# Kernel optimization log

Hardware: AMD Instinct MI355X
Metric: run time of the kernel (lower is better)

## Reference

```python
import jax, jax.numpy as jnp
import numpy as np

B, S, M = 8, 2048, 256
D = 512          # input/memory feature dim
P = 512          # proj_dim
H = 8            # num_heads


def setup_inputs() -> dict:
    key = jax.random.key(0)
    ks = jax.random.split(key, 10)
    sc = 0.02
    return {
        "input_seq": jax.random.normal(ks[0], (B, S, D), jnp.float32),
        "memory_cells": jax.random.normal(ks[1], (B, M, D), jnp.float32),
        "Wk": jax.random.normal(ks[2], (D, P), jnp.float32) * sc,
        "bk": jnp.zeros((P,), jnp.float32),
        "Wv": jax.random.normal(ks[3], (D, P), jnp.float32) * sc,
        "bv": jnp.zeros((P,), jnp.float32),
        "Wq": jax.random.normal(ks[4], (H, D, P), jnp.float32) * sc,  # stacked per-head query Dense
        "bq": jnp.zeros((H, P), jnp.float32),
        "Wo": jax.random.normal(ks[5], (H * P, P), jnp.float32) * sc,
        "bo": jnp.zeros((P,), jnp.float32),
    }


def reference(input_seq, memory_cells, Wk, bk, Wv, bv, Wq, bq, Wo, bo):
    # shared key/value projections (multi-query: one K/V for all heads)
    ik = input_seq @ Wk + bk          # [B,S,P]
    mk = memory_cells @ Wk + bk       # [B,M,P]
    iv = input_seq @ Wv + bv          # [B,S,P]
    mv = memory_cells @ Wv + bv       # [B,M,P]

    # per-head queries from memory cells, all heads at once
    q = jnp.einsum('bmd,hdp->bhmp', memory_cells, Wq) + bq[None, :, None, :]  # [B,H,M,P]

    input_score = jnp.einsum('bhmp,bsp->bhms', q, ik)          # [B,H,M,S]
    self_score = jnp.sum(q * mk[:, None], axis=-1, keepdims=True)  # [B,H,M,1]
    score = jnp.concatenate([self_score, input_score], axis=-1)    # [B,H,M,S+1]
    score = score / jnp.sqrt(jnp.float32(P))
    attn = jax.nn.softmax(score, axis=-1)

    self_attn = attn[..., 0:1]                                  # [B,H,M,1]
    input_attn = attn[..., 1:]                                  # [B,H,M,S]
    val = jnp.einsum('bhms,bsp->bhmp', input_attn, iv) + self_attn * mv[:, None]

    # concat heads: [B,M,H*P]
    concat = jnp.transpose(val, (0, 2, 1, 3)).reshape(B, M, H * P)
    return concat @ Wo + bo           # [B,M,P]
```

## Files before the change

### kernel.cpp

```cpp
#include <hip/hip_runtime.h>

#define B_ 8
#define S_ 2048
#define M_ 256
#define D_ 512
#define P_ 512
#define H_ 8

#define SCALE 0.044194173824159216f

typedef __attribute__((ext_vector_type(8))) short bf16x8;
typedef __attribute__((ext_vector_type(4))) float f32x4;

static __device__ __forceinline__ float bf2f(short u) {
  union { float f; unsigned int i; } x;
  x.i = ((unsigned int)(unsigned short)u) << 16;
  return x.f;
}
static __device__ __forceinline__ short f2bf(float f) {
  union { float f; unsigned int i; } x;
  x.f = f;
  unsigned int r = (x.i + 0x7FFFu + ((x.i >> 16) & 1u)) >> 16;
  return (short)r;
}

static __device__ __forceinline__ void gll16(const short* g, short* l) {
  __builtin_amdgcn_global_load_lds(
      (const __attribute__((address_space(1))) void*)g,
      (__attribute__((address_space(3))) void*)l, 16, 0, 0);
}

#define LGKM_WAIT() asm volatile("s_waitcnt lgkmcnt(0)" ::: "memory")
#define VMLG_WAIT() asm volatile("s_waitcnt vmcnt(0) lgkmcnt(0)" ::: "memory")
#define RAW_BAR() do { asm volatile("" ::: "memory"); __builtin_amdgcn_s_barrier(); asm volatile("" ::: "memory"); } while (0)

__global__ __launch_bounds__(256) void cast_both(
    const float* __restrict__ inA, short* __restrict__ outA, int n4A,
    const float* __restrict__ inM, short* __restrict__ outM)
{
  int idx = blockIdx.x * 256 + threadIdx.x;
  const float* in = inA;
  short* out = outA;
  if (idx >= n4A) { idx -= n4A; in = inM; out = outM; }
  float4 v = ((const float4*)in)[idx];
  short o0 = f2bf(v.x), o1 = f2bf(v.y), o2 = f2bf(v.z), o3 = f2bf(v.w);
  uint2 pk;
  pk.x = (unsigned int)(unsigned short)o0 | ((unsigned int)(unsigned short)o1 << 16);
  pk.y = (unsigned int)(unsigned short)o2 | ((unsigned int)(unsigned short)o3 << 16);
  ((uint2*)out)[idx] = pk;
}

__global__ __launch_bounds__(256) void wtrans_all(
    const float* __restrict__ Wk, const float* __restrict__ Wv,
    const float* __restrict__ Wq,
    short* __restrict__ WkT, short* __restrict__ WvT, short* __restrict__ WqT)
{
  __shared__ float tile[32][33];
  const int t = threadIdx.x, tx = t & 31, ty = t >> 5;
  const int z = blockIdx.z;
  const float* inp;
  short* outp;
  if (z == 0)      { inp = Wk; outp = WkT; }
  else if (z == 1) { inp = Wv; outp = WvT; }
  else             { inp = Wq + (size_t)(z - 2) * 512 * 512;
                     outp = WqT + (size_t)(z - 2) * 512 * 512; }
  const int n0 = blockIdx.x * 32, k0 = blockIdx.y * 32;
#pragma unroll
  for (int i = 0; i < 4; ++i)
    tile[ty + 8 * i][tx] = inp[(size_t)(k0 + ty + 8 * i) * 512 + n0 + tx];
  __syncthreads();
#pragma unroll
  for (int i = 0; i < 4; ++i)
    outp[(size_t)(n0 + ty + 8 * i) * 512 + k0 + tx] = f2bf(tile[tx][ty + 8 * i]);
}

__global__ __launch_bounds__(256) void wtrans_wo(
    const float* __restrict__ in, short* __restrict__ out)
{
  __shared__ float tile[32][33];
  const int t = threadIdx.x, tx = t & 31, ty = t >> 5;
  const int n0 = blockIdx.x * 32, k0 = blockIdx.y * 32;
#pragma unroll
  for (int i = 0; i < 4; ++i)
    tile[ty + 8 * i][tx] = in[(size_t)(k0 + ty + 8 * i) * 512 + n0 + tx];
  __syncthreads();
#pragma unroll
  for (int i = 0; i < 4; ++i)
    out[(size_t)(n0 + ty + 8 * i) * 4096 + k0 + tx] = f2bf(tile[tx][ty + 8 * i]);
}

template<int MODE, int K, int N, int LDA, int LDB>
__global__ __launch_bounds__(256, 3) void gemm128(
    const short* __restrict__ Abase, const short* __restrict__ Bbase,
    const float* __restrict__ bias, void* __restrict__ Cv,
    const size_t aZ, const size_t bZ, const size_t cZ,
    float* __restrict__ Ls,
    const float* __restrict__ eselfp, const short* __restrict__ mvbp)
{
  __shared__ short As[4096];
  __shared__ short Bs[4096];
  const int t = threadIdx.x;
  const int w = t >> 6, lane = t & 63, qd = lane >> 4, ln = lane & 15;
  const int wm = (w & 1) * 64, wn = (w >> 1) * 64;

  const int n0 = blockIdx.x * 128;
  const int m0 = blockIdx.y * 128;
  const int z = blockIdx.z;
  const int bsel = z;

  const short* A  = Abase + (size_t)z * aZ;
  const short* Bp = Bbase + (size_t)bsel * bZ;

  const int rr = t >> 2, g0 = t & 3;
  const int gs0 = g0 ^ ((rr >> 1) & 3);
  const int gs1 = g0 ^ (((rr + 64) >> 1) & 3);
  const short* ga0 = A + (size_t)(m0 + rr) * LDA + gs0 * 8;
  const short* ga1 = A + (size_t)(m0 + rr + 64) * LDA + gs1 * 8;
  const short* gb0 = Bp + (size_t)(n0 + rr) * LDB + gs0 * 8;
  const short* gb1 = Bp + (size_t)(n0 + rr + 64) * LDB + gs1 * 8;

  int aoff[4], boff[4];
#pragma unroll
  for (int mt = 0; mt < 4; ++mt) {
    int r = wm + mt * 16 + ln;
    aoff[mt] = r * 32 + (qd ^ ((r >> 1) & 3)) * 8;
  }
#pragma unroll
  for (int nt = 0; nt < 4; ++nt) {
    int r = wn + nt * 16 + ln;
    boff[nt] = r * 32 + (qd ^ ((r >> 1) & 3)) * 8;
  }

  f32x4 acc[4][4];
#pragma unroll
  for (int mt = 0; mt < 4; ++mt)
#pragma unroll
    for (int nt = 0; nt < 4; ++nt) acc[mt][nt] = (f32x4){0.f, 0.f, 0.f, 0.f};

  for (int kc = 0; kc < K; kc += 32) {
    __syncthreads();
    gll16(ga0 + kc, &As[w * 512]);
    gll16(ga1 + kc, &As[2048 + w * 512]);
    gll16(gb0 + kc, &Bs[w * 512]);
    gll16(gb1 + kc, &Bs[2048 + w * 512]);
    __syncthreads();

    bf16x8 af[4], bfr[4];
#pragma unroll
    for (int mt = 0; mt < 4; ++mt) af[mt] = *(const bf16x8*)&As[aoff[mt]];
#pragma unroll
    for (int nt = 0; nt < 4; ++nt) bfr[nt] = *(const bf16x8*)&Bs[boff[nt]];
#pragma unroll
    for (int mt = 0; mt < 4; ++mt)
#pragma unroll
      for (int nt = 0; nt < 4; ++nt)
        acc[mt][nt] = __builtin_amdgcn_mfma_f32_16x16x32_bf16(af[mt], bfr[nt], acc[mt][nt], 0, 0, 0);
  }

  if constexpr (MODE == 5) {
#pragma unroll
    for (int nt = 0; nt < 4; ++nt) {
      const int col = n0 + wn + nt * 16 + ln;
#pragma unroll
      for (int mt = 0; mt < 4; ++mt)
#pragma unroll
        for (int r = 0; r < 4; ++r) {
          const int row = m0 + wm + mt * 16 + qd * 4 + r;
          ((float*)Cv)[(size_t)z * cZ + (size_t)row * N + col] = acc[mt][nt][r];
        }
    }
  } else {
#pragma unroll
    for (int nt = 0; nt < 4; ++nt) {
      const int col = n0 + wn + nt * 16 + ln;
      const float bc = bias[512 * z + col];
#pragma unroll
      for (int mt = 0; mt < 4; ++mt)
#pragma unroll
        for (int r = 0; r < 4; ++r) {
          const int row = m0 + wm + mt * 16 + qd * 4 + r;
          const int bidx = row >> 8, ml = row & 255;
          ((short*)Cv)[((size_t)(bidx * H_ + z) * M_ + ml) * N + col] = f2bf(acc[mt][nt][r] + bc);
        }
    }
  }
}

template<int NKT>
__global__ __launch_bounds__(256, 3) void qk128(
    const short* __restrict__ Abase, const short* __restrict__ Bbase,
    short* __restrict__ Eb, float* __restrict__ Ls)
{
  __shared__ short lds[16384];
  const int t = threadIdx.x;
  const int w = t >> 6, lane = t & 63, qd = lane >> 4, ln = lane & 15;
  const int wrp = w & 1, wcp = w >> 1;
  const int b = blockIdx.x;
  const int n0 = blockIdx.y * 128, m0 = blockIdx.z * 128;

  const short* A  = Abase + (size_t)b * (2048 * 512) + (size_t)m0 * 512;
  const short* Bp = Bbase + (size_t)b * (2048 * 512) + (size_t)n0 * 512;

  const int srow = t >> 2;
  const int scol = ((t & 3) ^ ((srow >> 1) & 3)) * 8;
  const short* gsA = A  + (size_t)srow * 512 + scol;
  const short* gsB = Bp + (size_t)srow * 512 + scol;

  auto stage = [&](const short* g, short* l) {
    gll16(g,            l + w * 512);
    gll16(g + 64 * 512, l + 2048 + w * 512);
  };

  const int fq = (qd ^ ((ln >> 1) & 3)) * 8;
  int aoff[4], boff[4];
#pragma unroll
  for (int mt = 0; mt < 4; ++mt) aoff[mt] = (wrp * 64 + mt * 16 + ln) * 32 + fq;
#pragma unroll
  for (int nt = 0; nt < 4; ++nt) boff[nt] = (wcp * 64 + nt * 16 + ln) * 32 + fq;

  f32x4 acc[4][4];
#pragma unroll
  for (int i = 0; i < 4; ++i)
#pragma unroll
    for (int j = 0; j < 4; ++j) acc[i][j] = (f32x4){0.f, 0.f, 0.f, 0.f};

  stage(gsA, &lds[0]);
  stage(gsB, &lds[8192]);
  asm volatile("s_waitcnt vmcnt(0)" ::: "memory");
  __builtin_amdgcn_s_barrier();

#pragma unroll 1
  for (int kt = 0; kt < NKT; ++kt) {
    const int p = kt & 1;
    short* Ah = &lds[p * 4096];
    short* Bh = &lds[8192 + p * 4096];

    bf16x8 a[4], bfr[4];
#pragma unroll
    for (int nt = 0; nt < 4; ++nt) bfr[nt] = *(const bf16x8*)&Bh[boff[nt]];
#pragma unroll
    for (int mt = 0; mt < 4; ++mt) a[mt] = *(const bf16x8*)&Ah[aoff[mt]];

    if (kt + 1 < NKT) {
      stage(gsA + (size_t)(kt + 1) * 32, &lds[(p ^ 1) * 4096]);
      stage(gsB + (size_t)(kt + 1) * 32, &lds[8192 + (p ^ 1) * 4096]);
    }

    __builtin_amdgcn_s_setprio(1);
#pragma unroll
    for (int mt = 0; mt < 4; ++mt)
#pragma unroll
      for (int nt = 0; nt < 4; ++nt)
        acc[mt][nt] = __builtin_amdgcn_mfma_f32_16x16x32_bf16(a[mt], bfr[nt], acc[mt][nt], 0, 0, 0);
    __builtin_amdgcn_s_setprio(0);

    VMLG_WAIT();
    RAW_BAR();
  }

#pragma unroll
  for (int i = 0; i < 4; ++i)
#pragma unroll
    for (int j = 0; j < 4; ++j)
#pragma unroll
      for (int r = 0; r < 4; ++r)
        acc[i][j][r] = __expf(acc[i][j][r] * SCALE);
#pragma unroll
  for (int i = 0; i < 4; ++i)
#pragma unroll
    for (int r = 0; r < 4; ++r) {
      float rs = acc[i][0][r] + acc[i][1][r] + acc[i][2][r] + acc[i][3][r];
      rs += __shfl_xor(rs, 1);
      rs += __shfl_xor(rs, 2);
      rs += __shfl_xor(rs, 4);
      rs += __shfl_xor(rs, 8);
      if (ln == 0) {
        const int row = m0 + wrp * 64 + i * 16 + qd * 4 + r;
        atomicAdd(&Ls[(size_t)b * 2048 + row], rs);
      }
    }
#pragma unroll
  for (int i = 0; i < 4; ++i)
#pragma unroll
    for (int j = 0; j < 4; ++j)
#pragma unroll
      for (int r = 0; r < 4; ++r) {
        const int row = wrp * 64 + i * 16 + qd * 4 + r;
        const int col = wcp * 64 + j * 16 + ln;
        lds[row * 128 + (col ^ ((row & 7) << 3))] = f2bf(acc[i][j][r]);
      }
  LGKM_WAIT();
  RAW_BAR();
  short* Cb = Eb + (size_t)b * 2048 * 2048;
#pragma unroll
  for (int it = 0; it < 8; ++it) {
    const int flat = it * 256 + t;
    const int row = flat >> 4, c = flat & 15;
    bf16x8 v = *(const bf16x8*)&lds[row * 128 + ((c ^ (row & 7)) * 8)];
    *(bf16x8*)(Cb + (size_t)(m0 + row) * 2048 + n0 + c * 8) = v;
  }
}

template<int NKT>
__global__ __launch_bounds__(256, 3) void pv64(
    const short* __restrict__ Abase, const short* __restrict__ Bbase,
    short* __restrict__ valb, const float* __restrict__ Ls,
    const float* __restrict__ eselfp, const short* __restrict__ mvbp)
{
  __shared__ short lds[24576];
  const int t = threadIdx.x;
  const int w = t >> 6, lane = t & 63, qd = lane >> 4, ln = lane & 15;
  const int wrp = w & 1, wcp = w >> 1;
  const int b = blockIdx.x;
  const int n0 = blockIdx.y * 64;
  const int m0 = blockIdx.z * 128;

  const short* A  = Abase + (size_t)b * (2048 * 2048) + (size_t)m0 * 2048;
  const short* Bp = Bbase + (size_t)b * (512 * 2048) + (size_t)n0 * 2048;

  const int rr = t >> 3;
  const int sc = ((t & 7) ^ (rr & 7)) * 8;
  const short* gsA = A  + (size_t)rr * 2048 + sc;
  const short* gsB = Bp + (size_t)rr * 2048 + sc;

  auto stageA = [&](const short* g, short* l) {
#pragma unroll
    for (int kq = 0; kq < 4; ++kq)
      gll16(g + (size_t)(32 * kq) * 2048, l + kq * 2048 + w * 512);
  };
  auto stageB = [&](const short* g, short* l) {
#pragma unroll
    for (int kq = 0; kq < 2; ++kq)
      gll16(g + (size_t)(32 * kq) * 2048, l + kq * 2048 + w * 512);
  };

  const int cq0 = ((qd    ) ^ (ln & 7)) * 8;
  const int cq1 = ((4 + qd) ^ (ln & 7)) * 8;

  f32x4 acc[4][2];
#pragma unroll
  for (int i = 0; i < 4; ++i)
#pragma unroll
    for (int j = 0; j < 2; ++j) acc[i][j] = (f32x4){0.f, 0.f, 0.f, 0.f};

  stageA(gsA, &lds[0]);
  stageB(gsB, &lds[16384]);
  asm volatile("s_waitcnt vmcnt(0)" ::: "memory");
  __builtin_amdgcn_s_barrier();

#pragma unroll 1
  for (int kt = 0; kt < NKT; ++kt) {
    const int p = kt & 1;
    short* Ah = &lds[p * 8192 + wrp * 4096];
    short* Bh = &lds[16384 + p * 4096 + wcp * 2048];

    bf16x8 a[4][2], bfr[2][2];
#pragma unroll
    for (int nt = 0; nt < 2; ++nt) {
      bfr[nt][0] = *(const bf16x8*)&Bh[(nt * 16 + ln) * 64 + cq0];
      bfr[nt][1] = *(const bf16x8*)&Bh[(nt * 16 + ln) * 64 + cq1];
    }
#pragma unroll
    for (int mt = 0; mt < 4; ++mt) {
      a[mt][0] = *(const bf16x8*)&Ah[(mt * 16 + ln) * 64 + cq0];
      a[mt][1] = *(const bf16x8*)&Ah[(mt * 16 + ln) * 64 + cq1];
    }

    if (kt + 1 < NKT) {
      stageA(gsA + (size_t)(kt + 1) * 64, &lds[(p ^ 1) * 8192]);
      stageB(gsB + (size_t)(kt + 1) * 64, &lds[16384 + (p ^ 1) * 4096]);
    }

    __builtin_amdgcn_s_setprio(1);
#pragma unroll
    for (int kk = 0; kk < 2; ++kk)
#pragma unroll
      for (int mt = 0; mt < 4; ++mt)
#pragma unroll
        for (int nt = 0; nt < 2; ++nt)
          acc[mt][nt] = __builtin_amdgcn_mfma_f32_16x16x32_bf16(a[mt][kk], bfr[nt][kk], acc[mt][nt], 0, 0, 0);
    __builtin_amdgcn_s_setprio(0);

    VMLG_WAIT();
    RAW_BAR();
  }

#pragma unroll
  for (int mt = 0; mt < 4; ++mt)
#pragma unroll
    for (int r = 0; r < 4; ++r) {
      const int rl = wrp * 64 + mt * 16 + qd * 4 + r;
      const int R = m0 + rl;
      const float es  = eselfp[(size_t)b * 2048 + R];
      const float inv = 1.f / (es + Ls[(size_t)b * 2048 + R]);
      const short* mvr = mvbp + ((size_t)(b * 256 + (R & 255))) * 512;
#pragma unroll
      for (int j = 0; j < 2; ++j) {
        const int lcol = wcp * 32 + j * 16 + ln;
        const float v = (acc[mt][j][r] + es * bf2f(mvr[n0 + lcol])) * inv;
        lds[rl * 64 + (lcol ^ ((rl & 7) << 3))] = f2bf(v);
      }
    }
  LGKM_WAIT();
  RAW_BAR();
#pragma unroll
  for (int it = 0; it < 4; ++it) {
    const int flat = it * 256 + t;
    const int row = flat >> 3, c = flat & 7;
    const int R = m0 + row;
    bf16x8 v = *(const bf16x8*)&lds[row * 64 + ((c ^ (row & 7)) * 8)];
    *(bf16x8*)(valb + ((size_t)(b * 256 + (R & 255))) * 4096
               + (size_t)(R >> 8) * 512 + n0 + c * 8) = v;
  }
}

template<bool TRANSV>
__global__ __launch_bounds__(256, 3) void proj_kv(
    const short* __restrict__ A,
    const short* __restrict__ WkT, const short* __restrict__ WvT,
    const float* __restrict__ bk, const float* __restrict__ bv,
    short* __restrict__ Ck, short* __restrict__ Cvv)
{
  __shared__ short Sh[8192];
  short* As  = Sh;
  short* Bks = Sh + 4096;
  short* Bvs = Sh + 6144;
  const int t = threadIdx.x;
  const int w = t >> 6, lane = t & 63, qd = lane >> 4, ln = lane & 15;
  const int n0 = blockIdx.x * 64, m0 = blockIdx.y * 128;
  const int wm = (w & 1) * 64, wn2 = (w >> 1) * 32;

  const int rr = t >> 2, g0 = t & 3;
  const int gs0 = g0 ^ ((rr >> 1) & 3);
  const int gs1 = g0 ^ (((rr + 64) >> 1) & 3);
  const short* ga0 = A + (size_t)(m0 + rr) * 512 + gs0 * 8;
  const short* ga1 = A + (size_t)(m0 + rr + 64) * 512 + gs1 * 8;
  const short* gbk = WkT + (size_t)(n0 + rr) * 512 + gs0 * 8;
  const short* gbv = WvT + (size_t)(n0 + rr) * 512 + gs0 * 8;

  int aoff[4], boff[2];
#pragma unroll
  for (int mt = 0; mt < 4; ++mt) {
    int r = wm + mt * 16 + ln;
    aoff[mt] = r * 32 + (qd ^ ((r >> 1) & 3)) * 8;
  }
#pragma unroll
  for (int nt = 0; nt < 2; ++nt) {
    int r = wn2 + nt * 16 + ln;
    boff[nt] = r * 32 + (qd ^ ((r >> 1) & 3)) * 8;
  }

  f32x4 accK[4][2], accV[4][2];
#pragma unroll
  for (int mt = 0; mt < 4; ++mt)
#pragma unroll
    for (int nt = 0; nt < 2; ++nt) {
      accK[mt][nt] = (f32x4){0.f, 0.f, 0.f, 0.f};
      accV[mt][nt] = (f32x4){0.f, 0.f, 0.f, 0.f};
    }

  for (int kc = 0; kc < 512; kc += 32) {
    __syncthreads();
    gll16(ga0 + kc, &As[w * 512]);
    gll16(ga1 + kc, &As[2048 + w * 512]);
    gll16(gbk + kc, &Bks[w * 512]);
    gll16(gbv + kc, &Bvs[w * 512]);
    __syncthreads();

    bf16x8 af[4], bkf[2], bvf[2];
#pragma unroll
    for (int mt = 0; mt < 4; ++mt) af[mt] = *(const bf16x8*)&As[aoff[mt]];
#pragma unroll
    for (int nt = 0; nt < 2; ++nt) {
      bkf[nt] = *(const bf16x8*)&Bks[boff[nt]];
      bvf[nt] = *(const bf16x8*)&Bvs[boff[nt]];
    }
#pragma unroll
    for (int mt = 0; mt < 4; ++mt)
#pragma unroll
      for (int nt = 0; nt < 2; ++nt) {
        accK[mt][nt] = __builtin_amdgcn_mfma_f32_16x16x32_bf16(af[mt], bkf[nt], accK[mt][nt], 0, 0, 0);
        accV[mt][nt] = __builtin_amdgcn_mfma_f32_16x16x32_bf16(af[mt], bvf[nt], accV[mt][nt], 0, 0, 0);
      }
  }

#pragma unroll
  for (int nt = 0; nt < 2; ++nt) {
    const int col = n0 + wn2 + nt * 16 + ln;
    const float bc = bk[col];
#pragma unroll
    for (int mt = 0; mt < 4; ++mt)
#pragma unroll
      for (int r = 0; r < 4; ++r) {
        const int row = m0 + wm + mt * 16 + qd * 4 + r;
        Ck[(size_t)row * 512 + col] = f2bf(accK[mt][nt][r] + bc);
      }
  }

  if constexpr (!TRANSV) {
#pragma unroll
    for (int nt = 0; nt < 2; ++nt) {
      const int col = n0 + wn2 + nt * 16 + ln;
      const float bc = bv[col];
#pragma unroll
      for (int mt = 0; mt < 4; ++mt)
#pragma unroll
        for (int r = 0; r < 4; ++r) {
          const int row = m0 + wm + mt * 16 + qd * 4 + r;
          Cvv[(size_t)row * 512 + col] = f2bf(accV[mt][nt][r] + bc);
        }
    }
  } else {
    __syncthreads();
    short* ep = &Sh[w * 1280];
    const int lr = lane >> 1, lc16 = (lane & 1) * 16;
#pragma unroll
    for (int pass = 0; pass < 2; ++pass) {
#pragma unroll
      for (int mh = 0; mh < 2; ++mh) {
        const int mt = pass * 2 + mh;
#pragma unroll
        for (int nt = 0; nt < 2; ++nt) {
          const float bc = bv[n0 + wn2 + nt * 16 + ln];
#pragma unroll
          for (int r = 0; r < 4; ++r)
            ep[(nt * 16 + ln) * 40 + mh * 16 + qd * 4 + r] = f2bf(accV[mt][nt][r] + bc);
        }
      }
      LGKM_WAIT();
      const int srow0 = m0 + wm + pass * 32;
      const int bidx = srow0 >> 11;
      const int sloc = (srow0 & 2047) + lc16;
      const int pcol = n0 + wn2 + lr;
      short* outp = Cvv + (size_t)bidx * P_ * S_ + (size_t)pcol * S_ + sloc;
      *(bf16x8*)outp = *(const bf16x8*)&ep[lr * 40 + lc16];
      *(bf16x8*)(outp + 8) = *(const bf16x8*)&ep[lr * 40 + lc16 + 8];
      LGKM_WAIT();
    }
  }
}

__global__ __launch_bounds__(256) void reduce_wo(
    const float* __restrict__ partial, const float* __restrict__ bo,
    float* __restrict__ out)
{
  const int idx4 = blockIdx.x * 256 + threadIdx.x;
  float4 s = ((const float4*)bo)[idx4 & 127];
#pragma unroll
  for (int zz = 0; zz < 4; ++zz) {
    float4 p = ((const float4*)partial)[(size_t)zz * 262144 + idx4];
    s.x += p.x; s.y += p.y; s.z += p.z; s.w += p.w;
  }
  ((float4*)out)[idx4] = s;
}

__global__ __launch_bounds__(256) void selfscore(
    const short* __restrict__ qb, const short* __restrict__ mkb,
    float* __restrict__ eself, float* __restrict__ Ls)
{
  const int z = blockIdx.x, t = threadIdx.x;
  const short* qr = qb + ((size_t)z * M_ + t) * P_;
  const short* mr = mkb + ((size_t)(z >> 3) * M_ + t) * P_;
  float s = 0.f;
#pragma unroll 8
  for (int c = 0; c < P_; c += 8) {
    bf16x8 qv = *(const bf16x8*)(qr + c);
    bf16x8 mv = *(const bf16x8*)(mr + c);
#pragma unroll
    for (int j = 0; j < 8; ++j) s += bf2f(qv[j]) * bf2f(mv[j]);
  }
  eself[(size_t)z * M_ + t] = __expf(s * SCALE);
  Ls[(size_t)z * M_ + t] = 0.f;
}

extern "C" void kernel_launch(void* const* d_in, const int* in_sizes, int n_in,
                              void* d_out, int out_size, void* d_ws, size_t ws_size,
                              hipStream_t stream) {
  const float* input_seq = (const float*)d_in[0];
  const float* memcells  = (const float*)d_in[1];
  const float* Wk = (const float*)d_in[2];
  const float* bk = (const float*)d_in[3];
  const float* Wv = (const float*)d_in[4];
  const float* bv = (const float*)d_in[5];
  const float* Wq = (const float*)d_in[6];
  const float* bq = (const float*)d_in[7];
  const float* Wo = (const float*)d_in[8];
  const float* bo = (const float*)d_in[9];
  float* out = (float*)d_out;

  short* ws = (short*)d_ws;
  size_t o = 0;
  short* valb = ws + o; o += (size_t)B_ * M_ * H_ * P_;
  short* WoT  = ws + o; o += (size_t)(H_ * P_) * P_;
  short* mvb  = ws + o; o += (size_t)B_ * M_ * P_;
  short* mkb  = ws + o; o += (size_t)B_ * M_ * P_;
  short* qb   = ws + o; o += (size_t)B_ * H_ * M_ * P_;
  short* ivT  = ws + o; o += (size_t)B_ * P_ * S_;
  short* ikb  = ws + o; o += (size_t)B_ * S_ * P_;
  float* partial = (float*)(ws + o); o += (size_t)B_ * H_ * M_ * P_;
  float* eself = (float*)(ws + o); o += 2 * (size_t)B_ * H_ * M_;
  float* Ls    = (float*)(ws + o); o += 2 * (size_t)B_ * H_ * M_;
  short* region2 = ws + o;
  short* Ab  = region2;
  short* Mb  = Ab + (size_t)B_ * S_ * D_;
  short* WkT = Mb + (size_t)B_ * M_ * D_;
  short* WvT = WkT + (size_t)D_ * P_;
  short* WqT = WvT + (size_t)D_ * P_;
  short* Eb  = region2;

  dim3 blk(256);

  const int n4A = B_ * S_ * D_ / 4;
  const int n4M = B_ * M_ * D_ / 4;
  cast_both<<<dim3((n4A + n4M) / 256), blk, 0, stream>>>(input_seq, Ab, n4A, memcells, Mb);
  wtrans_all<<<dim3(16, 16, 10), blk, 0, stream>>>(Wk, Wv, Wq, WkT, WvT, WqT);
  wtrans_wo<<<dim3(16, 128), blk, 0, stream>>>(Wo, WoT);

  proj_kv<true><<<dim3(8, 128), blk, 0, stream>>>(Ab, WkT, WvT, bk, bv, ikb, ivT);
  proj_kv<false><<<dim3(8, 16), blk, 0, stream>>>(Mb, WkT, WvT, bk, bv, mkb, mvb);

  gemm128<1, 512, 512, 512, 512><<<dim3(4, 16, 8), blk, 0, stream>>>(
      Mb, WqT, bq, qb, 0, (size_t)D_ * P_, 0, nullptr, nullptr, nullptr);

  selfscore<<<dim3(64), blk, 0, stream>>>(qb, mkb, eself, Ls);

  qk128<16><<<dim3(8, 16, 16), blk, 0, stream>>>(qb, ikb, Eb, Ls);

  pv64<32><<<dim3(8, 8, 16), blk, 0, stream>>>(Eb, ivT, valb, Ls, eself, mvb);

  gemm128<5, 1024, 512, 4096, 4096><<<dim3(4, 16, 4), blk, 0, stream>>>(
      valb, WoT, nullptr, partial, 1024, 1024,
      (size_t)2048 * 512, nullptr, nullptr, nullptr);
  reduce_wo<<<dim3(1024), blk, 0, stream>>>(partial, bo, out);
}
```

Before: 321.0 us.

## Unify QK and PV GEMMs into a 4-stage pipelined kernel with register prefetch

Replaces the separate qk128 and pv64 kernels with one templated gemm7 kernel. It uses a 4-deep LDS ring of global-to-LDS loads kept three tiles ahead, and ping-pong register fragments so the next tile's LDS reads overlap the current tile's MFMAs. PV moves from 128x64 to 128x128 tiles with K-step 32, giving more reuse per block. The cost is double the LDS (64KB) and occupancy dropped from 3 to 2 blocks per CU, which may reduce latency hiding.

```diff
diff --git a/kernel.cpp b/kernel.cpp
--- a/kernel.cpp
+++ b/kernel.cpp
@@ -31,7 +31,6 @@
 }
 
 #define LGKM_WAIT() asm volatile("s_waitcnt lgkmcnt(0)" ::: "memory")
-#define VMLG_WAIT() asm volatile("s_waitcnt vmcnt(0) lgkmcnt(0)" ::: "memory")
 #define RAW_BAR() do { asm volatile("" ::: "memory"); __builtin_amdgcn_s_barrier(); asm volatile("" ::: "memory"); } while (0)
 
 __global__ __launch_bounds__(256) void cast_both(
@@ -186,29 +185,37 @@
   }
 }
 
-template<int NKT>
-__global__ __launch_bounds__(256, 3) void qk128(
+template<int NKT, int MODE, int LDA, int LDB>
+__global__ __launch_bounds__(256, 2) void gemm7(
     const short* __restrict__ Abase, const short* __restrict__ Bbase,
-    short* __restrict__ Eb, float* __restrict__ Ls)
-{
-  __shared__ short lds[16384];
+    short* __restrict__ Cb, float* __restrict__ Ls,
+    const float* __restrict__ eselfp, const short* __restrict__ mvbp,
+    const size_t aZ, const size_t bZ)
+{
+  __shared__ short lds[32768];
   const int t = threadIdx.x;
   const int w = t >> 6, lane = t & 63, qd = lane >> 4, ln = lane & 15;
   const int wrp = w & 1, wcp = w >> 1;
   const int b = blockIdx.x;
   const int n0 = blockIdx.y * 128, m0 = blockIdx.z * 128;
 
-  const short* A  = Abase + (size_t)b * (2048 * 512) + (size_t)m0 * 512;
-  const short* Bp = Bbase + (size_t)b * (2048 * 512) + (size_t)n0 * 512;
+  const short* A  = Abase + (size_t)b * aZ + (size_t)m0 * LDA;
+  const short* Bp = Bbase + (size_t)b * bZ + (size_t)n0 * LDB;
 
   const int srow = t >> 2;
   const int scol = ((t & 3) ^ ((srow >> 1) & 3)) * 8;
-  const short* gsA = A  + (size_t)srow * 512 + scol;
-  const short* gsB = Bp + (size_t)srow * 512 + scol;
-
-  auto stage = [&](const short* g, short* l) {
-    gll16(g,            l + w * 512);
-    gll16(g + 64 * 512, l + 2048 + w * 512);
+  const short* gsA = A  + (size_t)srow * LDA + scol;
+  const short* gsB = Bp + (size_t)srow * LDB + scol;
+
+  auto stageT = [&](int kt) {
+    short* la = &lds[(kt & 3) * 4096];
+    short* lb = &lds[16384 + (kt & 3) * 4096];
+    const short* ga = gsA + (size_t)kt * 32;
+    const short* gb = gsB + (size_t)kt * 32;
+    gll16(ga, la + w * 512);
+    gll16(ga + (size_t)64 * LDA, la + 2048 + w * 512);
+    gll16(gb, lb + w * 512);
+    gll16(gb + (size_t)64 * LDB, lb + 2048 + w * 512);
   };
 
   const int fq = (qd ^ ((ln >> 1) & 3)) * 8;
@@ -224,193 +231,121 @@
 #pragma unroll
     for (int j = 0; j < 4; ++j) acc[i][j] = (f32x4){0.f, 0.f, 0.f, 0.f};
 
-  stage(gsA, &lds[0]);
-  stage(gsB, &lds[8192]);
-  asm volatile("s_waitcnt vmcnt(0)" ::: "memory");
+  bf16x8 aX[4], bX[4], aY[4], bY[4];
+
+  stageT(0); stageT(1); stageT(2);
+  asm volatile("s_waitcnt vmcnt(4)" ::: "memory");
   __builtin_amdgcn_s_barrier();
+  {
+    const short* Ah = &lds[0];
+    const short* Bh = &lds[16384];
+#pragma unroll
+    for (int nt = 0; nt < 4; ++nt) bX[nt] = *(const bf16x8*)&Bh[boff[nt]];
+#pragma unroll
+    for (int mt = 0; mt < 4; ++mt) aX[mt] = *(const bf16x8*)&Ah[aoff[mt]];
+  }
+
+  auto iter = [&](int kt, bf16x8 (&ca)[4], bf16x8 (&cb)[4],
+                  bf16x8 (&na)[4], bf16x8 (&nb)[4]) {
+    if (kt + 1 < NKT) {
+      const short* Ah = &lds[((kt + 1) & 3) * 4096];
+      const short* Bh = &lds[16384 + ((kt + 1) & 3) * 4096];
+#pragma unroll
+      for (int nt = 0; nt < 4; ++nt) nb[nt] = *(const bf16x8*)&Bh[boff[nt]];
+#pragma unroll
+      for (int mt = 0; mt < 4; ++mt) na[mt] = *(const bf16x8*)&Ah[aoff[mt]];
+    }
+    if (kt + 3 < NKT) stageT(kt + 3);
+    __builtin_amdgcn_sched_barrier(0);
+    __builtin_amdgcn_s_setprio(1);
+#pragma unroll
+    for (int mt = 0; mt < 4; ++mt)
+#pragma unroll
+      for (int nt = 0; nt < 4; ++nt)
+        acc[mt][nt] = __builtin_amdgcn_mfma_f32_16x16x32_bf16(ca[mt], cb[nt], acc[mt][nt], 0, 0, 0);
+    __builtin_amdgcn_s_setprio(0);
+    asm volatile("s_waitcnt lgkmcnt(0)" ::: "memory");
+    if (kt + 3 < NKT) { asm volatile("s_waitcnt vmcnt(4)" ::: "memory"); }
+    else              { asm volatile("s_waitcnt vmcnt(0)" ::: "memory"); }
+    RAW_BAR();
+  };
 
 #pragma unroll 1
-  for (int kt = 0; kt < NKT; ++kt) {
-    const int p = kt & 1;
-    short* Ah = &lds[p * 4096];
-    short* Bh = &lds[8192 + p * 4096];
-
-    bf16x8 a[4], bfr[4];
-#pragma unroll
-    for (int nt = 0; nt < 4; ++nt) bfr[nt] = *(const bf16x8*)&Bh[boff[nt]];
-#pragma unroll
-    for (int mt = 0; mt < 4; ++mt) a[mt] = *(const bf16x8*)&Ah[aoff[mt]];
-
-    if (kt + 1 < NKT) {
-      stage(gsA + (size_t)(kt + 1) * 32, &lds[(p ^ 1) * 4096]);
-      stage(gsB + (size_t)(kt + 1) * 32, &lds[8192 + (p ^ 1) * 4096]);
-    }
-
-    __builtin_amdgcn_s_setprio(1);
+  for (int kt = 0; kt < NKT; kt += 2) {
+    iter(kt,     aX, bX, aY, bY);
+    iter(kt + 1, aY, bY, aX, bX);
+  }
+
+  if constexpr (MODE == 2) {
+#pragma unroll
+    for (int i = 0; i < 4; ++i)
+#pragma unroll
+      for (int j = 0; j < 4; ++j)
+#pragma unroll
+        for (int r = 0; r < 4; ++r)
+          acc[i][j][r] = __expf(acc[i][j][r] * SCALE);
+#pragma unroll
+    for (int i = 0; i < 4; ++i)
+#pragma unroll
+      for (int r = 0; r < 4; ++r) {
+        float rs = acc[i][0][r] + acc[i][1][r] + acc[i][2][r] + acc[i][3][r];
+        rs += __shfl_xor(rs, 1);
+        rs += __shfl_xor(rs, 2);
+        rs += __shfl_xor(rs, 4);
+        rs += __shfl_xor(rs, 8);
+        if (ln == 0) {
+          const int row = m0 + wrp * 64 + i * 16 + qd * 4 + r;
+          atomicAdd(&Ls[(size_t)b * 2048 + row], rs);
+        }
+      }
+#pragma unroll
+    for (int i = 0; i < 4; ++i)
+#pragma unroll
+      for (int j = 0; j < 4; ++j)
+#pragma unroll
+        for (int r = 0; r < 4; ++r) {
+          const int row = wrp * 64 + i * 16 + qd * 4 + r;
+          const int col = wcp * 64 + j * 16 + ln;
+          lds[row * 128 + (col ^ ((row & 7) << 3))] = f2bf(acc[i][j][r]);
+        }
+    LGKM_WAIT();
+    RAW_BAR();
+    short* Co = Cb + (size_t)b * 2048 * 2048;
+#pragma unroll
+    for (int it = 0; it < 8; ++it) {
+      const int flat = it * 256 + t;
+      const int row = flat >> 4, c = flat & 15;
+      bf16x8 v = *(const bf16x8*)&lds[row * 128 + ((c ^ (row & 7)) * 8)];
+      *(bf16x8*)(Co + (size_t)(m0 + row) * 2048 + n0 + c * 8) = v;
+    }
+  } else {
 #pragma unroll
     for (int mt = 0; mt < 4; ++mt)
 #pragma unroll
-      for (int nt = 0; nt < 4; ++nt)
-        acc[mt][nt] = __builtin_amdgcn_mfma_f32_16x16x32_bf16(a[mt], bfr[nt], acc[mt][nt], 0, 0, 0);
-    __builtin_amdgcn_s_setprio(0);
-
-    VMLG_WAIT();
+      for (int r = 0; r < 4; ++r) {
+        const int rl = wrp * 64 + mt * 16 + qd * 4 + r;
+        const int R = m0 + rl;
+        const float es  = eselfp[(size_t)b * 2048 + R];
+        const float inv = 1.f / (es + Ls[(size_t)b * 2048 + R]);
+        const short* mvr = mvbp + ((size_t)(b * 256 + (R & 255))) * 512;
+#pragma unroll
+        for (int j = 0; j < 4; ++j) {
+          const int lcol = wcp * 64 + j * 16 + ln;
+          const float v = (acc[mt][j][r] + es * bf2f(mvr[n0 + lcol])) * inv;
+          lds[rl * 128 + (lcol ^ ((rl & 7) << 3))] = f2bf(v);
+        }
+      }
+    LGKM_WAIT();
     RAW_BAR();
-  }
-
-#pragma unroll
-  for (int i = 0; i < 4; ++i)
-#pragma unroll
-    for (int j = 0; j < 4; ++j)
-#pragma unroll
-      for (int r = 0; r < 4; ++r)
-        acc[i][j][r] = __expf(acc[i][j][r] * SCALE);
-#pragma unroll
-  for (int i = 0; i < 4; ++i)
-#pragma unroll
-    for (int r = 0; r < 4; ++r) {
-      float rs = acc[i][0][r] + acc[i][1][r] + acc[i][2][r] + acc[i][3][r];
-      rs += __shfl_xor(rs, 1);
-      rs += __shfl_xor(rs, 2);
-      rs += __shfl_xor(rs, 4);
-      rs += __shfl_xor(rs, 8);
-      if (ln == 0) {
-        const int row = m0 + wrp * 64 + i * 16 + qd * 4 + r;
-        atomicAdd(&Ls[(size_t)b * 2048 + row], rs);
-      }
-    }
-#pragma unroll
-  for (int i = 0; i < 4; ++i)
-#pragma unroll
-    for (int j = 0; j < 4; ++j)
-#pragma unroll
-      for (int r = 0; r < 4; ++r) {
-        const int row = wrp * 64 + i * 16 + qd * 4 + r;
-        const int col = wcp * 64 + j * 16 + ln;
-        lds[row * 128 + (col ^ ((row & 7) << 3))] = f2bf(acc[i][j][r]);
-      }
-  LGKM_WAIT();
-  RAW_BAR();
-  short* Cb = Eb + (size_t)b * 2048 * 2048;
-#pragma unroll
-  for (int it = 0; it < 8; ++it) {
-    const int flat = it * 256 + t;
-    const int row = flat >> 4, c = flat & 15;
-    bf16x8 v = *(const bf16x8*)&lds[row * 128 + ((c ^ (row & 7)) * 8)];
-    *(bf16x8*)(Cb + (size_t)(m0 + row) * 2048 + n0 + c * 8) = v;
-  }
-}
-
-template<int NKT>
-__global__ __launch_bounds__(256, 3) void pv64(
-    const short* __restrict__ Abase, const short* __restrict__ Bbase,
-    short* __restrict__ valb, const float* __restrict__ Ls,
-    const float* __restrict__ eselfp, const short* __restrict__ mvbp)
-{
-  __shared__ short lds[24576];
-  const int t = threadIdx.x;
-  const int w = t >> 6, lane = t & 63, qd = lane >> 4, ln = lane & 15;
-  const int wrp = w & 1, wcp = w >> 1;
-  const int b = blockIdx.x;
-  const int n0 = blockIdx.y * 64;
-  const int m0 = blockIdx.z * 128;
-
-  const short* A  = Abase + (size_t)b * (2048 * 2048) + (size_t)m0 * 2048;
-  const short* Bp = Bbase + (size_t)b * (512 * 2048) + (size_t)n0 * 2048;
-
-  const int rr = t >> 3;
-  const int sc = ((t & 7) ^ (rr & 7)) * 8;
-  const short* gsA = A  + (size_t)rr * 2048 + sc;
-  const short* gsB = Bp + (size_t)rr * 2048 + sc;
-
-  auto stageA = [&](const short* g, short* l) {
-#pragma unroll
-    for (int kq = 0; kq < 4; ++kq)
-      gll16(g + (size_t)(32 * kq) * 2048, l + kq * 2048 + w * 512);
-  };
-  auto stageB = [&](const short* g, short* l) {
-#pragma unroll
-    for (int kq = 0; kq < 2; ++kq)
-      gll16(g + (size_t)(32 * kq) * 2048, l + kq * 2048 + w * 512);
-  };
-
-  const int cq0 = ((qd    ) ^ (ln & 7)) * 8;
-  const int cq1 = ((4 + qd) ^ (ln & 7)) * 8;
-
-  f32x4 acc[4][2];
-#pragma unroll
-  for (int i = 0; i < 4; ++i)
-#pragma unroll
-    for (int j = 0; j < 2; ++j) acc[i][j] = (f32x4){0.f, 0.f, 0.f, 0.f};
-
-  stageA(gsA, &lds[0]);
-  stageB(gsB, &lds[16384]);
-  asm volatile("s_waitcnt vmcnt(0)" ::: "memory");
-  __builtin_amdgcn_s_barrier();
-
-#pragma unroll 1
-  for (int kt = 0; kt < NKT; ++kt) {
-    const int p = kt & 1;
-    short* Ah = &lds[p * 8192 + wrp * 4096];
-    short* Bh = &lds[16384 + p * 4096 + wcp * 2048];
-
-    bf16x8 a[4][2], bfr[2][2];
-#pragma unroll
-    for (int nt = 0; nt < 2; ++nt) {
-      bfr[nt][0] = *(const bf16x8*)&Bh[(nt * 16 + ln) * 64 + cq0];
-      bfr[nt][1] = *(const bf16x8*)&Bh[(nt * 16 + ln) * 64 + cq1];
-    }
-#pragma unroll
-    for (int mt = 0; mt < 4; ++mt) {
-      a[mt][0] = *(const bf16x8*)&Ah[(mt * 16 + ln) * 64 + cq0];
-      a[mt][1] = *(const bf16x8*)&Ah[(mt * 16 + ln) * 64 + cq1];
-    }
-
-    if (kt + 1 < NKT) {
-      stageA(gsA + (size_t)(kt + 1) * 64, &lds[(p ^ 1) * 8192]);
-      stageB(gsB + (size_t)(kt + 1) * 64, &lds[16384 + (p ^ 1) * 4096]);
-    }
-
-    __builtin_amdgcn_s_setprio(1);
-#pragma unroll
-    for (int kk = 0; kk < 2; ++kk)
-#pragma unroll
-      for (int mt = 0; mt < 4; ++mt)
-#pragma unroll
-        for (int nt = 0; nt < 2; ++nt)
-          acc[mt][nt] = __builtin_amdgcn_mfma_f32_16x16x32_bf16(a[mt][kk], bfr[nt][kk], acc[mt][nt], 0, 0, 0);
-    __builtin_amdgcn_s_setprio(0);
-
-    VMLG_WAIT();
-    RAW_BAR();
-  }
-
-#pragma unroll
-  for (int mt = 0; mt < 4; ++mt)
-#pragma unroll
-    for (int r = 0; r < 4; ++r) {
-      const int rl = wrp * 64 + mt * 16 + qd * 4 + r;
-      const int R = m0 + rl;
-      const float es  = eselfp[(size_t)b * 2048 + R];
-      const float inv = 1.f / (es + Ls[(size_t)b * 2048 + R]);
-      const short* mvr = mvbp + ((size_t)(b * 256 + (R & 255))) * 512;
-#pragma unroll
-      for (int j = 0; j < 2; ++j) {
-        const int lcol = wcp * 32 + j * 16 + ln;
-        const float v = (acc[mt][j][r] + es * bf2f(mvr[n0 + lcol])) * inv;
-        lds[rl * 64 + (lcol ^ ((rl & 7) << 3))] = f2bf(v);
-      }
-    }
-  LGKM_WAIT();
-  RAW_BAR();
-#pragma unroll
-  for (int it = 0; it < 4; ++it) {
-    const int flat = it * 256 + t;
-    const int row = flat >> 3, c = flat & 7;
-    const int R = m0 + row;
-    bf16x8 v = *(const bf16x8*)&lds[row * 64 + ((c ^ (row & 7)) * 8)];
-    *(bf16x8*)(valb + ((size_t)(b * 256 + (R & 255))) * 4096
-               + (size_t)(R >> 8) * 512 + n0 + c * 8) = v;
+#pragma unroll
+    for (int it = 0; it < 8; ++it) {
+      const int flat = it * 256 + t;
+      const int row = flat >> 4, c = flat & 15;
+      const int R = m0 + row;
+      bf16x8 v = *(const bf16x8*)&lds[row * 128 + ((c ^ (row & 7)) * 8)];
+      *(bf16x8*)(Cb + ((size_t)(b * 256 + (R & 255))) * 4096
+                 + (size_t)(R >> 8) * 512 + n0 + c * 8) = v;
+    }
   }
 }
 
@@ -624,9 +559,13 @@
 
   selfscore<<<dim3(64), blk, 0, stream>>>(qb, mkb, eself, Ls);
 
-  qk128<16><<<dim3(8, 16, 16), blk, 0, stream>>>(qb, ikb, Eb, Ls);
-
-  pv64<32><<<dim3(8, 8, 16), blk, 0, stream>>>(Eb, ivT, valb, Ls, eself, mvb);
+  gemm7<16, 2, 512, 512><<<dim3(8, 16, 16), blk, 0, stream>>>(
+      qb, ikb, Eb, Ls, nullptr, nullptr,
+      (size_t)2048 * 512, (size_t)2048 * 512);
+
+  gemm7<64, 3, 2048, 2048><<<dim3(8, 4, 16), blk, 0, stream>>>(
+      Eb, ivT, valb, Ls, eself, mvb,
+      (size_t)2048 * 2048, (size_t)512 * 2048);
 
   gemm128<5, 1024, 512, 4096, 4096><<<dim3(4, 16, 4), blk, 0, stream>>>(
       valb, WoT, nullptr, partial, 1024, 1024,
```

Result: no change. 325.8 us (+1.5%).
